# Kernel optimization log

Hardware: AMD Instinct MI355X
Metric: run time of the kernel (lower is better)

Reference implementation:

```python
import jax, jax.numpy as jnp
import numpy as np

C = 256
NUM_HEADS = 4
HEAD_DIM = C // NUM_HEADS
GROUPS = 32
EPS = 1e-5


def setup_inputs() -> dict:
    key = jax.random.key(0)
    ks = jax.random.split(key, 7)
    B, H, W = 4, 64, 64
    x = jax.random.normal(ks[0], (B, C, H, W), dtype=jnp.float32)
    gn_w = jax.random.normal(ks[1], (C,), dtype=jnp.float32) * 0.02 + 1.0
    gn_b = jax.random.normal(ks[2], (C,), dtype=jnp.float32) * 0.02
    qkv_w = jax.random.normal(ks[3], (3 * C, C), dtype=jnp.float32) * (1.0 / np.sqrt(C))
    qkv_b = jax.random.normal(ks[4], (3 * C,), dtype=jnp.float32) * 0.02
    out_w = jax.random.normal(ks[5], (C, C), dtype=jnp.float32) * (1.0 / np.sqrt(C))
    out_b = jax.random.normal(ks[6], (C,), dtype=jnp.float32) * 0.02
    return {"x": x, "gn_w": gn_w, "gn_b": gn_b, "qkv_w": qkv_w,
            "qkv_b": qkv_b, "out_w": out_w, "out_b": out_b}


def _group_norm(x, w, b):
    # x: [B, C, H, W]; normalize over (C/GROUPS, H, W) per group
    B, Cc, Hh, Ww = x.shape
    xg = x.reshape(B, GROUPS, Cc // GROUPS, Hh, Ww)
    mean = jnp.mean(xg, axis=(2, 3, 4), keepdims=True)
    var = jnp.var(xg, axis=(2, 3, 4), keepdims=True)
    xg = (xg - mean) * jax.lax.rsqrt(var + EPS)
    xn = xg.reshape(B, Cc, Hh, Ww)
    return xn * w[None, :, None, None] + b[None, :, None, None]


def reference(x, gn_w, gn_b, qkv_w, qkv_b, out_w, out_b):
    B, Cc, Hh, Ww = x.shape
    N = Hh * Ww
    h = _group_norm(x, gn_w, gn_b).reshape(B, Cc, N)
    # qkv conv1d (kernel size 1) == pointwise linear over channel dim
    qkv = jnp.einsum('oc,bcn->bon', qkv_w, h) + qkv_b[None, :, None]
    q, k, v = jnp.split(qkv, 3, axis=1)
    q = q.reshape(B, NUM_HEADS, HEAD_DIM, N)
    k = k.reshape(B, NUM_HEADS, HEAD_DIM, N)
    v = v.reshape(B, NUM_HEADS, HEAD_DIM, N)
    scale = 1.0 / np.sqrt(HEAD_DIM)
    attn = jnp.einsum('bhdk,bhdl->bhkl', q, k) * scale  # [B, H, N, N]
    attn = jax.nn.softmax(attn, axis=-1)
    out = jnp.einsum('bhkl,bhdl->bhdk', attn, v)  # [B, H, D, N]
    out = out.reshape(B, Cc, N)
    out = jnp.einsum('oc,bcn->bon', out_w, out) + out_b[None, :, None]
    return x + out.reshape(B, Cc, Hh, Ww)
```

## Files before the change

### kernel.cpp

```cpp
#include <hip/hip_runtime.h>
#include <cstdint>

typedef __bf16 bf16_t;
typedef __bf16 bf16x4 __attribute__((ext_vector_type(4)));
typedef __bf16 bf16x8 __attribute__((ext_vector_type(8)));
typedef float f32x4 __attribute__((ext_vector_type(4)));
typedef unsigned int u32x2 __attribute__((ext_vector_type(2)));
typedef unsigned int u32x4 __attribute__((ext_vector_type(4)));

#define B_ 4
#define C_ 256
#define N_ 4096
#define NH_ 4
#define HD_ 64

static __device__ __forceinline__ f32x4 mfma_bf16(bf16x8 a, bf16x8 b, f32x4 c) {
  return __builtin_amdgcn_mfma_f32_16x16x32_bf16(a, b, c, 0, 0, 0);
}

static __device__ __forceinline__ void async16(const void* g, void* l) {
  __builtin_amdgcn_global_load_lds(
      (__attribute__((address_space(1))) void*)(uintptr_t)g,
      (__attribute__((address_space(3))) void*)(uint32_t)(uintptr_t)l,
      16, 0, 0);
}

static __device__ __forceinline__ float fexp2(float x) {
#if __has_builtin(__builtin_amdgcn_exp2f)
  return __builtin_amdgcn_exp2f(x);
#else
  return exp2f(x);
#endif
}

static __device__ __forceinline__ unsigned pack_bf16(float lo, float hi) {
  bf16x4 t;
  t[0] = (bf16_t)lo;
  t[1] = (bf16_t)hi;
  return *(unsigned*)&t;
}

__global__ __launch_bounds__(256) void k_gn_stats(const float* __restrict__ x,
                                                  const float* __restrict__ gn_w,
                                                  const float* __restrict__ gn_b,
                                                  float* __restrict__ gnscale,
                                                  float* __restrict__ gnshift) {
  const int bg = blockIdx.x;
  const int b = bg >> 5, g = bg & 31;
  const float4* p4 = (const float4*)(x + (size_t)(b * C_ + g * 8) * N_);
  float s = 0.f, ss = 0.f;
  for (int i = threadIdx.x; i < 8192; i += 256) {
    float4 v = p4[i];
    s += (v.x + v.y) + (v.z + v.w);
    ss += (v.x * v.x + v.y * v.y) + (v.z * v.z + v.w * v.w);
  }
  for (int off = 32; off > 0; off >>= 1) {
    s += __shfl_down(s, off);
    ss += __shfl_down(ss, off);
  }
  __shared__ float red_s[4], red_ss[4];
  const int wid = threadIdx.x >> 6, lane = threadIdx.x & 63;
  if (lane == 0) { red_s[wid] = s; red_ss[wid] = ss; }
  __syncthreads();
  if (threadIdx.x < 8) {
    float S = (red_s[0] + red_s[1]) + (red_s[2] + red_s[3]);
    float SS = (red_ss[0] + red_ss[1]) + (red_ss[2] + red_ss[3]);
    float mean = S * (1.f / 32768.f);
    float var = SS * (1.f / 32768.f) - mean * mean;
    float rstd = rsqrtf(var + 1e-5f);
    int c = g * 8 + threadIdx.x;
    float w = gn_w[c];
    gnscale[b * C_ + c] = w * rstd;
    gnshift[b * C_ + c] = gn_b[c] - mean * rstd * w;
  }
}

__global__ __launch_bounds__(256) void k_conv_w(const float* __restrict__ qkv_w,
                                                const float* __restrict__ out_w,
                                                bf16_t* __restrict__ w1,
                                                bf16_t* __restrict__ w2) {
  int i = blockIdx.x * 256 + threadIdx.x;
  if (i < 3 * C_ * C_) w1[i] = (bf16_t)qkv_w[i];
  else w2[i - 3 * C_ * C_] = (bf16_t)out_w[i - 3 * C_ * C_];
}

__global__ __launch_bounds__(256) void k_gn_apply(const float* __restrict__ x,
                                                  const float* __restrict__ gnscale,
                                                  const float* __restrict__ gnshift,
                                                  bf16_t* __restrict__ h) {
  const int chunk = blockIdx.x & 31;
  const int tok = (blockIdx.x >> 5) * 256 + threadIdx.x;
  const int b = tok >> 12, n = tok & (N_ - 1);
  const int c0 = chunk * 8;
  const float* xb = x + (size_t)(b * C_ + c0) * N_ + n;
  float sc[8], sh[8];
#pragma unroll
  for (int j = 0; j < 8; ++j) {
    sc[j] = gnscale[b * C_ + c0 + j];
    sh[j] = gnshift[b * C_ + c0 + j];
  }
  bf16x8 o;
#pragma unroll
  for (int j = 0; j < 8; ++j)
    o[j] = (bf16_t)(xb[(size_t)j * N_] * sc[j] + sh[j]);
  *(bf16x8*)(h + (size_t)tok * C_ + c0) = o;
}

__global__ __launch_bounds__(256) void k_gemm_qkv(const bf16_t* __restrict__ h,
                                                  const bf16_t* __restrict__ w1,
                                                  const float* __restrict__ qkv_b,
                                                  bf16_t* __restrict__ Qb,
                                                  bf16_t* __restrict__ Kb,
                                                  bf16_t* __restrict__ Vb) {
  __shared__ bf16_t As[128 * 32], Bs[128 * 32];
  const int tid = threadIdx.x, lane = tid & 63, wid = tid >> 6;
  const int g = lane >> 4, q = lane & 15;
  const int wm = wid >> 1, wn = wid & 1;
  const int m0 = blockIdx.x * 128;
  const int o0 = blockIdx.y * 128;
  f32x4 acc[4][4] = {};
  const int srow = lane >> 2, scol = (lane & 3) * 8;
  for (int kc = 0; kc < 8; ++kc) {
    const int k0 = kc * 32;
#pragma unroll
    for (int j = 0; j < 2; ++j) {
      const int chunk = wid + j * 4;
      async16(h + (size_t)(m0 + chunk * 16 + srow) * C_ + k0 + scol, &As[chunk * 512]);
      async16(w1 + (size_t)(o0 + chunk * 16 + srow) * C_ + k0 + scol, &Bs[chunk * 512]);
    }
    __syncthreads();
    bf16x8 a[4], bb[4];
#pragma unroll
    for (int t = 0; t < 4; ++t) {
      a[t] = *(const bf16x8*)&As[(wm * 64 + t * 16 + q) * 32 + g * 8];
      bb[t] = *(const bf16x8*)&Bs[(wn * 64 + t * 16 + q) * 32 + g * 8];
    }
#pragma unroll
    for (int mi = 0; mi < 4; ++mi)
#pragma unroll
      for (int ni = 0; ni < 4; ++ni)
        acc[mi][ni] = mfma_bf16(a[mi], bb[ni], acc[mi][ni]);
    __syncthreads();
  }
  const float QSCALE = 0.1803368801111244f;
#pragma unroll
  for (int ni = 0; ni < 4; ++ni) {
    const int o = o0 + wn * 64 + ni * 16 + q;
    const float bias = qkv_b[o];
    const int mat = o >> 8;
    const int c = o & 255, hh = c >> 6, d = c & 63;
#pragma unroll
    for (int mi = 0; mi < 4; ++mi) {
      const int tokb = m0 + wm * 64 + mi * 16 + g * 4;
      const int b = tokb >> 12, n = tokb & (N_ - 1);
      const size_t bh = (size_t)(b * NH_ + hh);
      f32x4 t = acc[mi][ni] + bias;
      if (mat == 0) {
#pragma unroll
        for (int r = 0; r < 4; ++r)
          Qb[(bh * N_ + n + r) * HD_ + d] = (bf16_t)(t[r] * QSCALE);
      } else if (mat == 1) {
#pragma unroll
        for (int r = 0; r < 4; ++r)
          Kb[(bh * N_ + n + r) * HD_ + d] = (bf16_t)t[r];
      } else {
        *(bf16x4*)(Vb + (bh * HD_ + d) * N_ + n) = __builtin_convertvector(t, bf16x4);
      }
    }
  }
}

template <int SPLIT>
__global__ __launch_bounds__(512) void k_attn(const bf16_t* __restrict__ Qb,
                                              const bf16_t* __restrict__ Kb,
                                              const bf16_t* __restrict__ Vb,
                                              bf16_t* __restrict__ att,
                                              bf16_t* __restrict__ Opart,
                                              float* __restrict__ lsum) {
  __shared__ __align__(16) bf16_t Ks[2][4096];
  __shared__ __align__(16) bf16_t Vs[2][4096];
  const int tid = threadIdx.x, lane = tid & 63, wid = tid >> 6;
  const int g = lane >> 4, q = lane & 15;
  const int qs = q & 7;
  int bid = blockIdx.x;
  const int nb = 256 * SPLIT;
  bid = (bid & 7) * (nb / 8) + (bid >> 3);
  int bh, qt, kh;
  if (SPLIT == 2) { bh = bid >> 5; qt = (bid >> 1) & 15; kh = bid & 1; }
  else { bh = bid >> 4; qt = bid & 15; kh = 0; }
  const int nq0 = qt * 256 + wid * 32;
  const int k00 = kh * (N_ / SPLIT);
  const int NT = (N_ / SPLIT) / 64;
  const size_t base = (size_t)bh << 18;
  const bf16_t* Qp = Qb + base;
  const bf16_t* Kp = Kb + base;
  const bf16_t* Vp = Vb + base;

  const bf16x8 bqA0 = *(const bf16x8*)(Qp + (size_t)(nq0 + q) * HD_ + g * 8);
  const bf16x8 bqA1 = *(const bf16x8*)(Qp + (size_t)(nq0 + q) * HD_ + 32 + g * 8);
  const bf16x8 bqB0 = *(const bf16x8*)(Qp + (size_t)(nq0 + 16 + q) * HD_ + g * 8);
  const bf16x8 bqB1 = *(const bf16x8*)(Qp + (size_t)(nq0 + 16 + q) * HD_ + 32 + g * 8);

  const int srow = lane >> 3;
  const int sc16 = (lane & 7) ^ srow;

  f32x4 laccA = {}, laccB = {};
  f32x4 accA[4] = {}, accB[4] = {};
  bf16x8 ones;
#pragma unroll
  for (int i = 0; i < 8; ++i) ones[i] = (bf16_t)1.0f;

  async16(Kp + (size_t)(k00 + wid * 8 + srow) * HD_ + sc16 * 8, &Ks[0][wid * 512]);
  async16(Vp + (size_t)(wid * 8 + srow) * N_ + k00 + sc16 * 8, &Vs[0][wid * 512]);
  __syncthreads();

  const bf16_t* kS = Kp + (size_t)(k00 + 64 + wid * 8 + srow) * HD_ + sc16 * 8;
  const bf16_t* vS = Vp + (size_t)(wid * 8 + srow) * N_ + k00 + 64 + sc16 * 8;

  for (int t = 0; t < NT; ++t) {
    const int buf = t & 1;
    if (t < NT - 1) {
      async16(kS, &Ks[buf ^ 1][wid * 512]);
      async16(vS, &Vs[buf ^ 1][wid * 512]);
      kS += 64 * HD_;
      vS += 64;
    }
    const bf16_t* Kl = Ks[buf];
    const bf16_t* Vl = Vs[buf];
    f32x4 z = {0.f, 0.f, 0.f, 0.f};
    f32x4 sA[4], sB[4];
    __builtin_amdgcn_s_setprio(1);
#pragma unroll
    for (int kb = 0; kb < 4; ++kb) {
      bf16x8 k0 = *(const bf16x8*)(Kl + (kb * 16 + q) * 64 + ((g ^ qs) * 8));
      bf16x8 k1 = *(const bf16x8*)(Kl + (kb * 16 + q) * 64 + (((4 + g) ^ qs) * 8));
      sA[kb] = mfma_bf16(k0, bqA0, z);
      sB[kb] = mfma_bf16(k0, bqB0, z);
      sA[kb] = mfma_bf16(k1, bqA1, sA[kb]);
      sB[kb] = mfma_bf16(k1, bqB1, sB[kb]);
    }
    __builtin_amdgcn_s_setprio(0);
#pragma unroll
    for (int kb = 0; kb < 4; ++kb)
#pragma unroll
      for (int r = 0; r < 4; ++r) {
        sA[kb][r] = fexp2(sA[kb][r]);
        sB[kb][r] = fexp2(sB[kb][r]);
      }
    bf16x8 pbA[2], pbB[2];
#pragma unroll
    for (int s = 0; s < 2; ++s) {
      const f32x4* st = s ? sB : sA;
      bf16x8* pb = s ? pbB : pbA;
#pragma unroll
      for (int h = 0; h < 2; ++h) {
        unsigned u0 = pack_bf16(st[2 * h][0], st[2 * h][1]);
        unsigned u1 = pack_bf16(st[2 * h][2], st[2 * h][3]);
        unsigned u2 = pack_bf16(st[2 * h + 1][0], st[2 * h + 1][1]);
        unsigned u3 = pack_bf16(st[2 * h + 1][2], st[2 * h + 1][3]);
        u32x4 w;
#if __has_builtin(__builtin_amdgcn_permlane32_swap) && __has_builtin(__builtin_amdgcn_permlane16_swap)
        u32x2 a02 = __builtin_amdgcn_permlane32_swap(u0, u2, false, false);
        u32x2 r02 = __builtin_amdgcn_permlane16_swap(a02[0], a02[1], false, false);
        u32x2 a13 = __builtin_amdgcn_permlane32_swap(u1, u3, false, false);
        u32x2 r13 = __builtin_amdgcn_permlane16_swap(a13[0], a13[1], false, false);
        w[0] = r02[0]; w[2] = r02[1]; w[1] = r13[0]; w[3] = r13[1];
#else
        const int sl0 = (g & 1) * 32 + q, sl1 = sl0 + 16;
        w[0] = (g < 2) ? __shfl((int)u0, sl0) : __shfl((int)u2, sl0);
        w[1] = (g < 2) ? __shfl((int)u1, sl0) : __shfl((int)u3, sl0);
        w[2] = (g < 2) ? __shfl((int)u0, sl1) : __shfl((int)u2, sl1);
        w[3] = (g < 2) ? __shfl((int)u1, sl1) : __shfl((int)u3, sl1);
#endif
        pb[h] = *(bf16x8*)&w;
      }
    }
    __builtin_amdgcn_s_setprio(1);
    laccA = mfma_bf16(ones, pbA[0], laccA);
    laccA = mfma_bf16(ones, pbA[1], laccA);
    laccB = mfma_bf16(ones, pbB[0], laccB);
    laccB = mfma_bf16(ones, pbB[1], laccB);
#pragma unroll
    for (int db = 0; db < 4; ++db) {
      bf16x8 v0 = *(const bf16x8*)(Vl + (db * 16 + q) * 64 + ((g ^ qs) * 8));
      bf16x8 v1 = *(const bf16x8*)(Vl + (db * 16 + q) * 64 + (((4 + g) ^ qs) * 8));
      accA[db] = mfma_bf16(v0, pbA[0], accA[db]);
      accB[db] = mfma_bf16(v0, pbB[0], accB[db]);
      accA[db] = mfma_bf16(v1, pbA[1], accA[db]);
      accB[db] = mfma_bf16(v1, pbB[1], accB[db]);
    }
    __builtin_amdgcn_s_setprio(0);
    __syncthreads();
  }

  if (SPLIT == 1) {
    const float invA = 1.0f / laccA[0], invB = 1.0f / laccB[0];
    const int b = bh >> 2, hh = bh & 3;
    bf16_t* opA = att + ((size_t)b * N_ + nq0 + q) * C_ + hh * HD_;
    bf16_t* opB = att + ((size_t)b * N_ + nq0 + 16 + q) * C_ + hh * HD_;
#pragma unroll
    for (int db = 0; db < 4; ++db) {
      f32x4 va = accA[db] * invA;
      f32x4 vb = accB[db] * invB;
      *(bf16x4*)(opA + db * 16 + g * 4) = __builtin_convertvector(va, bf16x4);
      *(bf16x4*)(opB + db * 16 + g * 4) = __builtin_convertvector(vb, bf16x4);
    }
  } else {
    bf16_t* opA = Opart + ((size_t)(kh * 16 + bh) * N_ + nq0 + q) * HD_;
    bf16_t* opB = opA + 16 * HD_;
#pragma unroll
    for (int db = 0; db < 4; ++db) {
      *(bf16x4*)(opA + db * 16 + g * 4) = __builtin_convertvector(accA[db], bf16x4);
      *(bf16x4*)(opB + db * 16 + g * 4) = __builtin_convertvector(accB[db], bf16x4);
    }
    if (g == 0) {
      const size_t mlb = (size_t)(kh * 16 + bh) * N_;
      lsum[mlb + nq0 + q] = laccA[0];
      lsum[mlb + nq0 + 16 + q] = laccB[0];
    }
  }
}

__global__ __launch_bounds__(256) void k_attn_combine(const bf16_t* __restrict__ Opart,
                                                      const float* __restrict__ lsum,
                                                      bf16_t* __restrict__ att) {
  const int gid = blockIdx.x * 256 + threadIdx.x;
  const int d8 = gid & 7;
  const int q = (gid >> 3) & (N_ - 1);
  const int bh = gid >> 15;
  const float l1 = lsum[(size_t)bh * N_ + q];
  const float l2 = lsum[(size_t)(16 + bh) * N_ + q];
  const float inv = 1.0f / (l1 + l2);
  const bf16x8 o1 = *(const bf16x8*)(Opart + ((size_t)bh * N_ + q) * HD_ + d8 * 8);
  const bf16x8 o2 = *(const bf16x8*)(Opart + ((size_t)(16 + bh) * N_ + q) * HD_ + d8 * 8);
  bf16x8 r;
#pragma unroll
  for (int j = 0; j < 8; ++j)
    r[j] = (bf16_t)(((float)o1[j] + (float)o2[j]) * inv);
  const int b = bh >> 2, hh = bh & 3;
  *(bf16x8*)(att + ((size_t)b * N_ + q) * C_ + hh * HD_ + d8 * 8) = r;
}

__global__ __launch_bounds__(256) void k_gemm_out(const bf16_t* __restrict__ att,
                                                  const bf16_t* __restrict__ w2,
                                                  const float* __restrict__ out_b,
                                                  const float* __restrict__ x,
                                                  float* __restrict__ out) {
  __shared__ bf16_t As[128 * 32], Bs[128 * 32];
  const int tid = threadIdx.x, lane = tid & 63, wid = tid >> 6;
  const int g = lane >> 4, q = lane & 15;
  const int wm = wid >> 1, wn = wid & 1;
  const int m0 = blockIdx.x * 128;
  const int o0 = blockIdx.y * 128;
  f32x4 acc[4][4] = {};
  const int srow = lane >> 2, scol = (lane & 3) * 8;
  for (int kc = 0; kc < 8; ++kc) {
    const int k0 = kc * 32;
#pragma unroll
    for (int j = 0; j < 2; ++j) {
      const int chunk = wid + j * 4;
      async16(att + (size_t)(m0 + chunk * 16 + srow) * C_ + k0 + scol, &As[chunk * 512]);
      async16(w2 + (size_t)(o0 + chunk * 16 + srow) * C_ + k0 + scol, &Bs[chunk * 512]);
    }
    __syncthreads();
    bf16x8 a[4], bb[4];
#pragma unroll
    for (int t = 0; t < 4; ++t) {
      a[t] = *(const bf16x8*)&As[(wm * 64 + t * 16 + q) * 32 + g * 8];
      bb[t] = *(const bf16x8*)&Bs[(wn * 64 + t * 16 + q) * 32 + g * 8];
    }
#pragma unroll
    for (int mi = 0; mi < 4; ++mi)
#pragma unroll
      for (int ni = 0; ni < 4; ++ni)
        acc[mi][ni] = mfma_bf16(a[mi], bb[ni], acc[mi][ni]);
    __syncthreads();
  }
#pragma unroll
  for (int ni = 0; ni < 4; ++ni) {
    const int o = o0 + wn * 64 + ni * 16 + q;
    const float bias = out_b[o];
#pragma unroll
    for (int mi = 0; mi < 4; ++mi) {
      const int tokb = m0 + wm * 64 + mi * 16 + g * 4;
      const int b = tokb >> 12, n = tokb & (N_ - 1);
      const size_t idx = ((size_t)(b * C_ + o) << 12) + n;
      const float4 xv = *(const float4*)(x + idx);
      f32x4 t = acc[mi][ni];
      float4 r = make_float4(t[0] + bias + xv.x, t[1] + bias + xv.y,
                             t[2] + bias + xv.z, t[3] + bias + xv.w);
      *(float4*)(out + idx) = r;
    }
  }
}

extern "C" void kernel_launch(void* const* d_in, const int* in_sizes, int n_in,
                              void* d_out, int out_size, void* d_ws, size_t ws_size,
                              hipStream_t stream) {
  (void)in_sizes; (void)n_in; (void)out_size;
  const float* x = (const float*)d_in[0];
  const float* gn_w = (const float*)d_in[1];
  const float* gn_b = (const float*)d_in[2];
  const float* qkv_w = (const float*)d_in[3];
  const float* qkv_b = (const float*)d_in[4];
  const float* out_w = (const float*)d_in[5];
  const float* out_b = (const float*)d_in[6];
  float* out = (float*)d_out;

  char* ws = (char*)d_ws;
  float* gnscale = (float*)ws;
  float* gnshift = gnscale + 1024;
  bf16_t* w1bf = (bf16_t*)(ws + 8192);
  bf16_t* w2bf = w1bf + 196608;
  bf16_t* hbuf = w2bf + 65536;
  bf16_t* Qb = hbuf + 4194304;
  bf16_t* Kb = Qb + 4194304;
  bf16_t* Vb = Kb + 4194304;
  bf16_t* Opart = Vb + 4194304;
  float* lsum = (float*)(Opart + 8388608);
  const size_t need = (size_t)((char*)(lsum + 131072) - ws);
  const bool split = ws_size >= need;

  k_gn_stats<<<128, 256, 0, stream>>>(x, gn_w, gn_b, gnscale, gnshift);
  k_conv_w<<<1024, 256, 0, stream>>>(qkv_w, out_w, w1bf, w2bf);
  k_gn_apply<<<2048, 256, 0, stream>>>(x, gnscale, gnshift, hbuf);
  k_gemm_qkv<<<dim3(128, 6), 256, 0, stream>>>(hbuf, w1bf, qkv_b, Qb, Kb, Vb);
  if (split) {
    k_attn<2><<<512, 512, 0, stream>>>(Qb, Kb, Vb, hbuf, Opart, lsum);
    k_attn_combine<<<2048, 256, 0, stream>>>(Opart, lsum, hbuf);
  } else {
    k_attn<1><<<256, 512, 0, stream>>>(Qb, Kb, Vb, hbuf, Opart, lsum);
  }
  k_gemm_out<<<dim3(128, 2), 256, 0, stream>>>(hbuf, w2bf, out_b, x, out);
}
```

Measured before the change: 128.1 us.

## Switch attention kernel to 32x32x16 MFMA tiles with VALU row-sum

The attention inner loop moves from 16x16x32 MFMA tiles to 32x32x16 tiles, which changes the register layout of scores, probabilities and accumulators. The P-matrix reshuffle needs only permlane32_swap instead of a 32+16 swap pair. The softmax denominator is now summed with VALU adds plus one cross-lane shuffle rather than extra MFMAs against a ones vector, and launch bounds request 4 blocks per CU. The intent is fewer MFMA instructions, fewer LDS reads and fewer permute operations per tile, at the risk of higher register pressure from the f32x16 accumulators.

```diff
diff --git a/kernel.cpp b/kernel.cpp
--- a/kernel.cpp
+++ b/kernel.cpp
@@ -5,6 +5,7 @@
 typedef __bf16 bf16x4 __attribute__((ext_vector_type(4)));
 typedef __bf16 bf16x8 __attribute__((ext_vector_type(8)));
 typedef float f32x4 __attribute__((ext_vector_type(4)));
+typedef float f32x16 __attribute__((ext_vector_type(16)));
 typedef unsigned int u32x2 __attribute__((ext_vector_type(2)));
 typedef unsigned int u32x4 __attribute__((ext_vector_type(4)));
 
@@ -16,6 +17,10 @@
 
 static __device__ __forceinline__ f32x4 mfma_bf16(bf16x8 a, bf16x8 b, f32x4 c) {
   return __builtin_amdgcn_mfma_f32_16x16x32_bf16(a, b, c, 0, 0, 0);
+}
+
+static __device__ __forceinline__ f32x16 mfma32(bf16x8 a, bf16x8 b, f32x16 c) {
+  return __builtin_amdgcn_mfma_f32_32x32x16_bf16(a, b, c, 0, 0, 0);
 }
 
 static __device__ __forceinline__ void async16(const void* g, void* l) {
@@ -171,17 +176,17 @@
 }
 
 template <int SPLIT>
-__global__ __launch_bounds__(512) void k_attn(const bf16_t* __restrict__ Qb,
-                                              const bf16_t* __restrict__ Kb,
-                                              const bf16_t* __restrict__ Vb,
-                                              bf16_t* __restrict__ att,
-                                              bf16_t* __restrict__ Opart,
-                                              float* __restrict__ lsum) {
+__global__ __launch_bounds__(512, 4) void k_attn(const bf16_t* __restrict__ Qb,
+                                                 const bf16_t* __restrict__ Kb,
+                                                 const bf16_t* __restrict__ Vb,
+                                                 bf16_t* __restrict__ att,
+                                                 bf16_t* __restrict__ Opart,
+                                                 float* __restrict__ lsum) {
   __shared__ __align__(16) bf16_t Ks[2][4096];
   __shared__ __align__(16) bf16_t Vs[2][4096];
   const int tid = threadIdx.x, lane = tid & 63, wid = tid >> 6;
-  const int g = lane >> 4, q = lane & 15;
-  const int qs = q & 7;
+  const int l31 = lane & 31, hi = lane >> 5;
+  const int r7 = l31 & 7;
   int bid = blockIdx.x;
   const int nb = 256 * SPLIT;
   bid = (bid & 7) * (nb / 8) + (bid >> 3);
@@ -196,19 +201,16 @@
   const bf16_t* Kp = Kb + base;
   const bf16_t* Vp = Vb + base;
 
-  const bf16x8 bqA0 = *(const bf16x8*)(Qp + (size_t)(nq0 + q) * HD_ + g * 8);
-  const bf16x8 bqA1 = *(const bf16x8*)(Qp + (size_t)(nq0 + q) * HD_ + 32 + g * 8);
-  const bf16x8 bqB0 = *(const bf16x8*)(Qp + (size_t)(nq0 + 16 + q) * HD_ + g * 8);
-  const bf16x8 bqB1 = *(const bf16x8*)(Qp + (size_t)(nq0 + 16 + q) * HD_ + 32 + g * 8);
+  bf16x8 bq[4];
+#pragma unroll
+  for (int i = 0; i < 4; ++i)
+    bq[i] = *(const bf16x8*)(Qp + (size_t)(nq0 + l31) * HD_ + i * 16 + hi * 8);
 
   const int srow = lane >> 3;
   const int sc16 = (lane & 7) ^ srow;
 
-  f32x4 laccA = {}, laccB = {};
-  f32x4 accA[4] = {}, accB[4] = {};
-  bf16x8 ones;
-#pragma unroll
-  for (int i = 0; i < 8; ++i) ones[i] = (bf16_t)1.0f;
+  f32x16 acc0 = {}, acc1 = {};
+  float lacc = 0.f;
 
   async16(Kp + (size_t)(k00 + wid * 8 + srow) * HD_ + sc16 * 8, &Ks[0][wid * 512]);
   async16(Vp + (size_t)(wid * 8 + srow) * N_ + k00 + sc16 * 8, &Vs[0][wid * 512]);
@@ -227,96 +229,108 @@
     }
     const bf16_t* Kl = Ks[buf];
     const bf16_t* Vl = Vs[buf];
-    f32x4 z = {0.f, 0.f, 0.f, 0.f};
-    f32x4 sA[4], sB[4];
+    f32x16 s0, s1;
+    const f32x16 z = {};
     __builtin_amdgcn_s_setprio(1);
 #pragma unroll
-    for (int kb = 0; kb < 4; ++kb) {
-      bf16x8 k0 = *(const bf16x8*)(Kl + (kb * 16 + q) * 64 + ((g ^ qs) * 8));
-      bf16x8 k1 = *(const bf16x8*)(Kl + (kb * 16 + q) * 64 + (((4 + g) ^ qs) * 8));
-      sA[kb] = mfma_bf16(k0, bqA0, z);
-      sB[kb] = mfma_bf16(k0, bqB0, z);
-      sA[kb] = mfma_bf16(k1, bqA1, sA[kb]);
-      sB[kb] = mfma_bf16(k1, bqB1, sB[kb]);
+    for (int i = 0; i < 4; ++i) {
+      bf16x8 k0 = *(const bf16x8*)(Kl + l31 * 64 + ((2 * i + hi) ^ r7) * 8);
+      bf16x8 k1 = *(const bf16x8*)(Kl + (32 + l31) * 64 + ((2 * i + hi) ^ r7) * 8);
+      if (i == 0) {
+        s0 = mfma32(k0, bq[0], z);
+        s1 = mfma32(k1, bq[0], z);
+      } else {
+        s0 = mfma32(k0, bq[i], s0);
+        s1 = mfma32(k1, bq[i], s1);
+      }
     }
     __builtin_amdgcn_s_setprio(0);
 #pragma unroll
-    for (int kb = 0; kb < 4; ++kb)
-#pragma unroll
-      for (int r = 0; r < 4; ++r) {
-        sA[kb][r] = fexp2(sA[kb][r]);
-        sB[kb][r] = fexp2(sB[kb][r]);
+    for (int r = 0; r < 16; ++r) {
+      s0[r] = fexp2(s0[r]);
+      s1[r] = fexp2(s1[r]);
+    }
+    float lt0 = 0.f, lt1 = 0.f;
+#pragma unroll
+    for (int r = 0; r < 16; ++r) {
+      lt0 += s0[r];
+      lt1 += s1[r];
+    }
+    lacc += lt0 + lt1;
+    bf16x8 pb[4];
+#pragma unroll
+    for (int kc = 0; kc < 4; ++kc) {
+      const int bs = (kc & 1) * 8;
+      unsigned uA, uB, uC, uD;
+      if (kc < 2) {
+        uA = pack_bf16(s0[bs + 0], s0[bs + 1]);
+        uB = pack_bf16(s0[bs + 2], s0[bs + 3]);
+        uC = pack_bf16(s0[bs + 4], s0[bs + 5]);
+        uD = pack_bf16(s0[bs + 6], s0[bs + 7]);
+      } else {
+        uA = pack_bf16(s1[bs + 0], s1[bs + 1]);
+        uB = pack_bf16(s1[bs + 2], s1[bs + 3]);
+        uC = pack_bf16(s1[bs + 4], s1[bs + 5]);
+        uD = pack_bf16(s1[bs + 6], s1[bs + 7]);
       }
-    bf16x8 pbA[2], pbB[2];
-#pragma unroll
-    for (int s = 0; s < 2; ++s) {
-      const f32x4* st = s ? sB : sA;
-      bf16x8* pb = s ? pbB : pbA;
-#pragma unroll
-      for (int h = 0; h < 2; ++h) {
-        unsigned u0 = pack_bf16(st[2 * h][0], st[2 * h][1]);
-        unsigned u1 = pack_bf16(st[2 * h][2], st[2 * h][3]);
-        unsigned u2 = pack_bf16(st[2 * h + 1][0], st[2 * h + 1][1]);
-        unsigned u3 = pack_bf16(st[2 * h + 1][2], st[2 * h + 1][3]);
-        u32x4 w;
-#if __has_builtin(__builtin_amdgcn_permlane32_swap) && __has_builtin(__builtin_amdgcn_permlane16_swap)
-        u32x2 a02 = __builtin_amdgcn_permlane32_swap(u0, u2, false, false);
-        u32x2 r02 = __builtin_amdgcn_permlane16_swap(a02[0], a02[1], false, false);
-        u32x2 a13 = __builtin_amdgcn_permlane32_swap(u1, u3, false, false);
-        u32x2 r13 = __builtin_amdgcn_permlane16_swap(a13[0], a13[1], false, false);
-        w[0] = r02[0]; w[2] = r02[1]; w[1] = r13[0]; w[3] = r13[1];
+      u32x4 w;
+#if __has_builtin(__builtin_amdgcn_permlane32_swap)
+      u32x2 sAC = __builtin_amdgcn_permlane32_swap(uA, uC, false, false);
+      u32x2 sBD = __builtin_amdgcn_permlane32_swap(uB, uD, false, false);
+      w[0] = sAC[0]; w[1] = sBD[0]; w[2] = sAC[1]; w[3] = sBD[1];
 #else
-        const int sl0 = (g & 1) * 32 + q, sl1 = sl0 + 16;
-        w[0] = (g < 2) ? __shfl((int)u0, sl0) : __shfl((int)u2, sl0);
-        w[1] = (g < 2) ? __shfl((int)u1, sl0) : __shfl((int)u3, sl0);
-        w[2] = (g < 2) ? __shfl((int)u0, sl1) : __shfl((int)u2, sl1);
-        w[3] = (g < 2) ? __shfl((int)u1, sl1) : __shfl((int)u3, sl1);
+      w[0] = (hi == 0) ? uA : (unsigned)__shfl((int)uC, l31);
+      w[1] = (hi == 0) ? uB : (unsigned)__shfl((int)uD, l31);
+      w[2] = (hi == 0) ? (unsigned)__shfl((int)uA, l31 + 32) : uC;
+      w[3] = (hi == 0) ? (unsigned)__shfl((int)uB, l31 + 32) : uD;
 #endif
-        pb[h] = *(bf16x8*)&w;
-      }
+      pb[kc] = *(bf16x8*)&w;
     }
     __builtin_amdgcn_s_setprio(1);
-    laccA = mfma_bf16(ones, pbA[0], laccA);
-    laccA = mfma_bf16(ones, pbA[1], laccA);
-    laccB = mfma_bf16(ones, pbB[0], laccB);
-    laccB = mfma_bf16(ones, pbB[1], laccB);
-#pragma unroll
-    for (int db = 0; db < 4; ++db) {
-      bf16x8 v0 = *(const bf16x8*)(Vl + (db * 16 + q) * 64 + ((g ^ qs) * 8));
-      bf16x8 v1 = *(const bf16x8*)(Vl + (db * 16 + q) * 64 + (((4 + g) ^ qs) * 8));
-      accA[db] = mfma_bf16(v0, pbA[0], accA[db]);
-      accB[db] = mfma_bf16(v0, pbB[0], accB[db]);
-      accA[db] = mfma_bf16(v1, pbA[1], accA[db]);
-      accB[db] = mfma_bf16(v1, pbB[1], accB[db]);
+#pragma unroll
+    for (int kc = 0; kc < 4; ++kc) {
+      bf16x8 v0 = *(const bf16x8*)(Vl + l31 * 64 + ((2 * kc + hi) ^ r7) * 8);
+      bf16x8 v1 = *(const bf16x8*)(Vl + (32 + l31) * 64 + ((2 * kc + hi) ^ r7) * 8);
+      acc0 = mfma32(v0, pb[kc], acc0);
+      acc1 = mfma32(v1, pb[kc], acc1);
     }
     __builtin_amdgcn_s_setprio(0);
     __syncthreads();
   }
 
+  lacc += __shfl_xor(lacc, 32);
+
   if (SPLIT == 1) {
-    const float invA = 1.0f / laccA[0], invB = 1.0f / laccB[0];
+    const float inv = 1.0f / lacc;
     const int b = bh >> 2, hh = bh & 3;
-    bf16_t* opA = att + ((size_t)b * N_ + nq0 + q) * C_ + hh * HD_;
-    bf16_t* opB = att + ((size_t)b * N_ + nq0 + 16 + q) * C_ + hh * HD_;
-#pragma unroll
-    for (int db = 0; db < 4; ++db) {
-      f32x4 va = accA[db] * invA;
-      f32x4 vb = accB[db] * invB;
-      *(bf16x4*)(opA + db * 16 + g * 4) = __builtin_convertvector(va, bf16x4);
-      *(bf16x4*)(opB + db * 16 + g * 4) = __builtin_convertvector(vb, bf16x4);
+    bf16_t* op = att + ((size_t)b * N_ + nq0 + l31) * C_ + hh * HD_;
+#pragma unroll
+    for (int dt = 0; dt < 2; ++dt) {
+      const f32x16& a = dt ? acc1 : acc0;
+#pragma unroll
+      for (int qd = 0; qd < 4; ++qd) {
+        bf16x4 r;
+#pragma unroll
+        for (int m = 0; m < 4; ++m) r[m] = (bf16_t)(a[qd * 4 + m] * inv);
+        *(bf16x4*)(op + dt * 32 + qd * 8 + hi * 4) = r;
+      }
     }
   } else {
-    bf16_t* opA = Opart + ((size_t)(kh * 16 + bh) * N_ + nq0 + q) * HD_;
-    bf16_t* opB = opA + 16 * HD_;
-#pragma unroll
-    for (int db = 0; db < 4; ++db) {
-      *(bf16x4*)(opA + db * 16 + g * 4) = __builtin_convertvector(accA[db], bf16x4);
-      *(bf16x4*)(opB + db * 16 + g * 4) = __builtin_convertvector(accB[db], bf16x4);
-    }
-    if (g == 0) {
+    bf16_t* op = Opart + ((size_t)(kh * 16 + bh) * N_ + nq0 + l31) * HD_;
+#pragma unroll
+    for (int dt = 0; dt < 2; ++dt) {
+      const f32x16& a = dt ? acc1 : acc0;
+#pragma unroll
+      for (int qd = 0; qd < 4; ++qd) {
+        bf16x4 r;
+#pragma unroll
+        for (int m = 0; m < 4; ++m) r[m] = (bf16_t)a[qd * 4 + m];
+        *(bf16x4*)(op + dt * 32 + qd * 8 + hi * 4) = r;
+      }
+    }
+    if (hi == 0) {
       const size_t mlb = (size_t)(kh * 16 + bh) * N_;
-      lsum[mlb + nq0 + q] = laccA[0];
-      lsum[mlb + nq0 + 16 + q] = laccB[0];
+      lsum[mlb + nq0 + l31] = lacc;
     }
   }
 }
```

After: 138.0 us. +7.8%, slower.
